# Performance work log

Hardware: AMD Instinct MI355X
Metric: run time of the kernel (lower is better)

Reference implementation:

```python
import jax, jax.numpy as jnp
import numpy as np

EPS_BN = 1e-5   # torch BatchNorm1d default eps
K = 3           # de_neighbors


def conv1(x, w):
    # 1x1 Conv1d, no bias: x [B,C,N], w [O,C] -> [B,O,N]
    return jnp.einsum('oc,bcn->bon', w, x)


def bn_relu(y, g, b):
    # BatchNorm1d in training mode (batch statistics, biased variance) + ReLU
    mean = jnp.mean(y, axis=(0, 2), keepdims=True)
    var = jnp.var(y, axis=(0, 2), keepdims=True)
    yn = (y - mean) * jax.lax.rsqrt(var + EPS_BN)
    return jax.nn.relu(yn * g[None, :, None] + b[None, :, None])


def propagate(xyz1, xyz2, p1, p2, k):
    # xyz1 [B,N,3] fine coords, xyz2 [B,S,3] coarse coords,
    # p1 [B,D1,N] fine feats, p2 [B,D2,S] coarse feats -> [B,D1+D2,N]
    pts2 = p2.transpose(0, 2, 1)  # [B,S,D2]
    # squared pairwise distances [B,N,S]
    d = (jnp.sum(xyz1 ** 2, -1)[:, :, None]
         + jnp.sum(xyz2 ** 2, -1)[:, None, :]
         - 2.0 * jnp.einsum('bnc,bsc->bns', xyz1, xyz2))
    negd, idx = jax.lax.top_k(-d, k)          # k smallest distances
    dists = -negd                              # [B,N,k]
    w = 1.0 / (dists + 1e-8)
    w = w / jnp.sum(w, -1, keepdims=True)      # inverse-distance weights
    B = xyz1.shape[0]
    gathered = pts2[jnp.arange(B)[:, None, None], idx]     # [B,N,k,D2]
    interp = jnp.sum(gathered * w[..., None], axis=2)      # [B,N,D2]
    new = jnp.concatenate([p1.transpose(0, 2, 1), interp], axis=-1)
    return new.transpose(0, 2, 1)


def setup_inputs() -> dict:
    key = jax.random.key(0)
    ks = jax.random.split(key, 20)
    B = 16
    npts = [2048, 512, 128, 32, 8]
    ch = [64, 128, 256, 512, 1024]
    inp = {}
    for i in range(5):
        inp[f'xyz{i}'] = jax.random.normal(ks[i], (B, npts[i], 3), jnp.float32)
        inp[f'x{i}'] = jax.random.normal(ks[5 + i], (B, ch[i], npts[i]), jnp.float32)
    lin_dims = [1536, 1792, 1920, 1984]
    for i, dmid in enumerate(lin_dims):
        inp[f'w_lin{i}'] = jax.random.normal(ks[10 + i], (dmid, dmid), jnp.float32) * (1.0 / np.sqrt(dmid))
        inp[f'g_lin{i}'] = jnp.ones((dmid,), jnp.float32)
        inp[f'b_lin{i}'] = jnp.zeros((dmid,), jnp.float32)
    inp['w_dec0'] = jax.random.normal(ks[14], (256, 1984), jnp.float32) * (1.0 / np.sqrt(1984))
    inp['g_dec'] = jnp.ones((256,), jnp.float32)
    inp['b_dec'] = jnp.zeros((256,), jnp.float32)
    inp['w_dec1'] = jax.random.normal(ks[15], (1, 256), jnp.float32) * (1.0 / np.sqrt(256))
    return inp


def reference(xyz0, xyz1, xyz2, xyz3, xyz4,
              x0, x1, x2, x3, x4,
              w_lin0, g_lin0, b_lin0,
              w_lin1, g_lin1, b_lin1,
              w_lin2, g_lin2, b_lin2,
              w_lin3, g_lin3, b_lin3,
              w_dec0, g_dec, b_dec, w_dec1):
    # lists are reversed in forward: coarsest first
    x = x4
    x = propagate(xyz3, xyz4, x3, x, K)   # [B,1536,32]
    x = bn_relu(conv1(x, w_lin0), g_lin0, b_lin0)
    x = propagate(xyz2, xyz3, x2, x, K)   # [B,1792,128]
    x = bn_relu(conv1(x, w_lin1), g_lin1, b_lin1)
    x = propagate(xyz1, xyz2, x1, x, K)   # [B,1920,512]
    x = bn_relu(conv1(x, w_lin2), g_lin2, b_lin2)
    x = propagate(xyz0, xyz1, x0, x, K)   # [B,1984,2048]
    x = bn_relu(conv1(x, w_lin3), g_lin3, b_lin3)
    # str_dec: Linear1Layer(1984,256) -> Dropout(eval=identity) -> Conv1d(256,1)
    x = bn_relu(conv1(x, w_dec0), g_dec, b_dec)
    out = conv1(x, w_dec1)                # [B,1,N]
    return out.squeeze(1)                 # [B,N]
```

## Files before the change

kernel.cpp:

```cpp
#include <hip/hip_runtime.h>
#include <stdint.h>
#include <stddef.h>

typedef _Float16 half8 __attribute__((ext_vector_type(8)));
typedef _Float16 half4v __attribute__((ext_vector_type(4)));
typedef float f32x4 __attribute__((ext_vector_type(4)));

__device__ __forceinline__ void gload_lds16(const void* g, void* l) {
  __builtin_amdgcn_global_load_lds((const __attribute__((address_space(1))) void*)g,
                                   (__attribute__((address_space(3))) void*)l, 16, 0, 0);
}

struct TPack {
  const float* in[5];
  _Float16* out[5];
  int C[5], N[5];
  int cum[6];
};
__global__ __launch_bounds__(256) void k_transpose_all(TPack p) {
  __shared__ float tile[32][33];
  int t = blockIdx.x;
  int ti = 0;
#pragma unroll
  for (int i = 0; i < 5; ++i) if (t >= p.cum[i + 1]) ti = i + 1;
// ... 16 lines not shown
  __syncthreads();
#pragma unroll
  for (int j = 0; j < 32; j += 8) {
    int n = n0 + ty + j, c = c0 + tx;
    if (n < N && c < C) out[((size_t)b * N + n) * C + c] = (_Float16)tile[tx][ty + j];
  }
}

__global__ __launch_bounds__(256) void k_cast_pad_w(const float* __restrict__ W,
                                                    _Float16* __restrict__ Wh,
                                                    int O, int K, int Opad, int Kpad) {
  size_t i = ((size_t)blockIdx.x * 256 + threadIdx.x) * 4;
  if (i >= (size_t)Opad * Kpad) return;
  int r = (int)(i / Kpad), k = (int)(i % Kpad);
  half4v v;
#pragma unroll
  for (int j = 0; j < 4; ++j) {
    float f = (r < O && (k + j) < K) ? W[(size_t)r * K + k + j] : 0.f;
    v[j] = (_Float16)f;
  }
  *(half4v*)(Wh + i) = v;
}

struct KPack {
  const float* q[4]; const float* p[4];
  int N1[4], S[4];
  int cum[5];
  int obase[4];
};
#define KNN_INS(dd, ii) { float _d = (dd); int _i = (ii); \
  if (_d < d0)      { d2 = d1; i2 = i1; d1 = d0; i1 = i0; d0 = _d; i0 = _i; } \
  else if (_d < d1) { d2 = d1; i2 = i1; d1 = _d; i1 = _i; } \
  else if (_d < d2) { d2 = _d; i2 = _i; } }
__global__ __launch_bounds__(256) void k_knn_all(KPack kp, int4* __restrict__ idxo,
                                                 float4* __restrict__ wo) {
  __shared__ float sp[512 * 3];
  __shared__ float spp[512];
  int t = blockIdx.x;
  int st = 0;
#pragma unroll
  for (int i = 0; i < 4; ++i) if (t >= kp.cum[i + 1]) st = i + 1;
  int lb = t - kp.cum[st];
  int N1 = kp.N1[st], S = kp.S[st];
  int nb = (N1 * 4 + 255) / 256;
  int b = lb / nb;
  int xb = lb - b * nb;
  const float* p = kp.p[st];
  const float* q = kp.q[st];
  for (int i = threadIdx.x; i < S * 3; i += 256) sp[i] = p[(size_t)b * S * 3 + i];
  __syncthreads();
  for (int s = threadIdx.x; s < S; s += 256)
    spp[s] = sp[s * 3] * sp[s * 3] + sp[s * 3 + 1] * sp[s * 3 + 1] + sp[s * 3 + 2] * sp[s * 3 + 2];
  __syncthreads();
  int tt = xb * 256 + threadIdx.x;
  int n = tt >> 2, sub = tt & 3;
  if (n >= N1) return;
  const float* qp = q + ((size_t)b * N1 + n) * 3;
  float qx = qp[0], qy = qp[1], qz = qp[2];
  float qq = qx * qx + qy * qy + qz * qz;
  float d0 = 1e30f, d1 = 1e30f, d2 = 1e30f;
  int i0 = 0, i1 = 0, i2 = 0;
  int Sq = S >> 2;
  int s0 = sub * Sq;
  for (int i = 0; i < Sq; ++i) {
    int s = s0 + i;
    float d = qq + spp[s] - 2.f * (qx * sp[s * 3] + qy * sp[s * 3 + 1] + qz * sp[s * 3 + 2]);
    KNN_INS(d, s);
  }
#pragma unroll
  for (int m = 1; m <= 2; m <<= 1) {
    float rd0 = __shfl_xor(d0, m, 64), rd1 = __shfl_xor(d1, m, 64), rd2 = __shfl_xor(d2, m, 64);
    int   ri0 = __shfl_xor(i0, m, 64), ri1 = __shfl_xor(i1, m, 64), ri2 = __shfl_xor(i2, m, 64);
    KNN_INS(rd0, ri0); KNN_INS(rd1, ri1); KNN_INS(rd2, ri2);
  }
  if (sub == 0) {
    float w0 = 1.f / (d0 + 1e-8f), w1 = 1.f / (d1 + 1e-8f), w2 = 1.f / (d2 + 1e-8f);
    float wsum = w0 + w1 + w2;
    int gi = kp.obase[st] + b * N1 + n;
    idxo[gi] = make_int4(b * S + i0, b * S + i1, b * S + i2, 0);
    wo[gi] = make_float4(w0 / wsum, w1 / wsum, w2 / wsum, 0.f);
  }
}

__global__ __launch_bounds__(256) void k_bn_norm(_Float16* __restrict__ G,
                                                 const float* __restrict__ scale,
                                                 const float* __restrict__ shiftv,
                                                 size_t total8, int ld) {
  size_t i = (size_t)blockIdx.x * 256 + threadIdx.x;
  if (i >= total8) return;
  half8 v = *(half8*)&G[i * 8];
  int c0 = (int)((i * 8) % (size_t)ld);
#pragma unroll
  for (int j = 0; j < 8; ++j) {
    float f = (float)v[j] * scale[c0 + j] + shiftv[c0 + j];
    v[j] = (_Float16)fmaxf(f, 0.f);
  }
  *(half8*)&G[i * 8] = v;
}


__global__ __launch_bounds__(256) void k_gemm_anorm(const _Float16* __restrict__ A,
                                                    const float* __restrict__ scale,
                                                    const float* __restrict__ shift,
                                                    int apply_nr,
                                                    const _Float16* __restrict__ W,
                                                    _Float16* __restrict__ Cout,
                                                    int K, int lda, int ldb, int ldc) {
  __shared__ __align__(16) _Float16 lA[128 * 64];
  __shared__ __align__(16) _Float16 lB[128 * 64];
  int tid = threadIdx.x;
  int m0 = blockIdx.x * 128;
  int o0 = blockIdx.y * 128;
  int lane = tid & 63, wv = tid >> 6;
  int wm = (wv & 1) * 64, wo = (wv >> 1) * 64;
  int lr = lane & 15, lq = lane >> 4;
  int trow = tid >> 3;
  int tsegl = (((tid & 7) ^ (trow & 7))) * 8;
  int sw = lr & 7;

  f32x4 acc[4][4];
#pragma unroll
  for (int mi = 0; mi < 4; ++mi)
#pragma unroll
    for (int oi = 0; oi < 4; ++oi)
      acc[mi][oi] = (f32x4){0.f, 0.f, 0.f, 0.f};

  const _Float16* gA = A + (size_t)(m0 + trow) * lda + tsegl;
  const _Float16* gB = W + (size_t)(o0 + trow) * ldb + tsegl;

  for (int k0 = 0; k0 < K; k0 += 64) {
#pragma unroll
    for (int i = 0; i < 4; ++i)
      gload_lds16(gB + (size_t)(32 * i) * ldb + k0, lB + ((size_t)i * 256 + tid) * 8);
    if (apply_nr) {
      float sc[8], sh[8];
#pragma unroll
      for (int j = 0; j < 8; ++j) { sc[j] = scale[k0 + tsegl + j]; sh[j] = shift[k0 + tsegl + j]; }
#pragma unroll
      for (int i = 0; i < 4; ++i) {
        half8 v = *(const half8*)(gA + (size_t)(32 * i) * lda + k0);
        half8 o;
#pragma unroll
        for (int j = 0; j < 8; ++j)
          o[j] = (_Float16)fmaxf((float)v[j] * sc[j] + sh[j], 0.f);
        *(half8*)&lA[((size_t)i * 256 + tid) * 8] = o;
      }
    } else {
#pragma unroll
      for (int i = 0; i < 4; ++i)
        gload_lds16(gA + (size_t)(32 * i) * lda + k0, lA + ((size_t)i * 256 + tid) * 8);
    }
    __syncthreads();
#pragma unroll
    for (int ks = 0; ks < 64; ks += 32) {
      half8 af[4], bf[4];
#pragma unroll
      for (int mi = 0; mi < 4; ++mi)
        af[mi] = *(const half8*)&lA[(wm + mi * 16 + lr) * 64 + ((((ks >> 3) + lq) ^ sw)) * 8];
#pragma unroll
      for (int oi = 0; oi < 4; ++oi)
        bf[oi] = *(const half8*)&lB[(wo + oi * 16 + lr) * 64 + ((((ks >> 3) + lq) ^ sw)) * 8];
#pragma unroll
      for (int mi = 0; mi < 4; ++mi)
#pragma unroll
        for (int oi = 0; oi < 4; ++oi)
          acc[mi][oi] = __builtin_amdgcn_mfma_f32_16x16x32_f16(af[mi], bf[oi], acc[mi][oi], 0, 0, 0);
    }
    __syncthreads();
  }

#pragma unroll
  for (int mi = 0; mi < 4; ++mi)
#pragma unroll
    for (int oi = 0; oi < 4; ++oi) {
      int col = o0 + wo + oi * 16 + lr;
      int rowb = m0 + wm + mi * 16 + lq * 4;
#pragma unroll
      for (int r = 0; r < 4; ++r)
        Cout[(size_t)(rowb + r) * ldc + col] = (_Float16)acc[mi][oi][r];
    }
}

__global__ __launch_bounds__(256) void k_gemm_yis(const _Float16* __restrict__ A,
                                                  const _Float16* __restrict__ W,
                                                  const _Float16* __restrict__ Z,
                                                  const int4* __restrict__ idxb,
                                                  const float4* __restrict__ wb,
                                                  _Float16* __restrict__ Y,
                                                  float* __restrict__ sum,
                                                  float* __restrict__ sumsq,
                                                  int K, int lda, int ldb, int ldy,
                                                  int ldz, int zcol0) {
  __shared__ __align__(16) _Float16 lsm[2 * 128 * 64];
  __shared__ int4 sIdx[128];
  __shared__ float4 sWt[128];
  __shared__ float sStat[256];
  _Float16* lA = lsm;
  _Float16* lB = lsm + 128 * 64;
  int tid = threadIdx.x;
  int m0 = blockIdx.x * 128;
  int o0 = blockIdx.y * 128;
  if (tid < 128) {
    sIdx[tid] = idxb[m0 + tid];
    sWt[tid] = wb[m0 + tid];
  }
  sStat[tid] = 0.f;
  int lane = tid & 63, wv = tid >> 6;
  int wm = (wv & 1) * 64, wo = (wv >> 1) * 64;
  int lr = lane & 15, lq = lane >> 4;
  int trow = tid >> 3;
  int tsegl = (((tid & 7) ^ (trow & 7))) * 8;
  int sw = lr & 7;

  f32x4 acc[4][4];
#pragma unroll
  for (int mi = 0; mi < 4; ++mi)
#pragma unroll
    for (int oi = 0; oi < 4; ++oi)
      acc[mi][oi] = (f32x4){0.f, 0.f, 0.f, 0.f};

  const _Float16* gA = A + (size_t)(m0 + trow) * lda + tsegl;
  const _Float16* gB = W + (size_t)(o0 + trow) * ldb + tsegl;

  for (int k0 = 0; k0 < K; k0 += 64) {
#pragma unroll
    for (int i = 0; i < 4; ++i) {
      gload_lds16(gA + (size_t)(32 * i) * lda + k0, lA + ((size_t)i * 256 + tid) * 8);
      gload_lds16(gB + (size_t)(32 * i) * ldb + k0, lB + ((size_t)i * 256 + tid) * 8);
    }
    __syncthreads();
#pragma unroll
    for (int ks = 0; ks < 64; ks += 32) {
      half8 af[4], bf[4];
#pragma unroll
      for (int mi = 0; mi < 4; ++mi)
        af[mi] = *(const half8*)&lA[(wm + mi * 16 + lr) * 64 + ((((ks >> 3) + lq) ^ sw)) * 8];
#pragma unroll
      for (int oi = 0; oi < 4; ++oi)
        bf[oi] = *(const half8*)&lB[(wo + oi * 16 + lr) * 64 + ((((ks >> 3) + lq) ^ sw)) * 8];
#pragma unroll
      for (int mi = 0; mi < 4; ++mi)
#pragma unroll
        for (int oi = 0; oi < 4; ++oi)
          acc[mi][oi] = __builtin_amdgcn_mfma_f32_16x16x32_f16(af[mi], bf[oi], acc[mi][oi], 0, 0, 0);
    }
    __syncthreads();
  }

#pragma unroll
  for (int mi = 0; mi < 4; ++mi)
#pragma unroll
    for (int oi = 0; oi < 4; ++oi)
#pragma unroll
      for (int r = 0; r < 4; ++r)
        lsm[(wm + mi * 16 + lq * 4 + r) * 128 + (wo + oi * 16 + lr)] = (_Float16)acc[mi][oi][r];
  __syncthreads();

  int tcol = (tid & 15) * 8;
  int rbase = tid >> 4;
  float s8[8], q8[8];
#pragma unroll
  for (int j = 0; j < 8; ++j) { s8[j] = 0.f; q8[j] = 0.f; }
#pragma unroll
  for (int i = 0; i < 8; ++i) {
    int row = rbase + i * 16;
    int4 id = sIdx[row];
    float4 w = sWt[row];
    half8 y = *(half8*)&lsm[row * 128 + tcol];
    int zc = zcol0 + o0 + tcol;
    half8 a  = *(const half8*)&Z[(size_t)id.x * ldz + zc];
    half8 b2 = *(const half8*)&Z[(size_t)id.y * ldz + zc];
    half8 c2 = *(const half8*)&Z[(size_t)id.z * ldz + zc];
    half8 o;
#pragma unroll
    for (int j = 0; j < 8; ++j) {
      float v = (float)y[j] + w.x * (float)a[j] + w.y * (float)b2[j] + w.z * (float)c2[j];
      o[j] = (_Float16)v;
      s8[j] += v; q8[j] += v * v;
    }
    *(half8*)&Y[(size_t)(m0 + row) * ldy + o0 + tcol] = o;
  }
#pragma unroll
  for (int j = 0; j < 8; ++j) {
    atomicAdd(&sStat[tcol + j], s8[j]);
    atomicAdd(&sStat[128 + tcol + j], q8[j]);
  }
  __syncthreads();
  if (tid < 128) {
    atomicAdd(&sum[o0 + tid], sStat[tid]);
    atomicAdd(&sumsq[o0 + tid], sStat[128 + tid]);
  }
}

__global__ __launch_bounds__(256) void k_gemm_dec_acc(const _Float16* __restrict__ A,
                                                      const float* __restrict__ sumc,
                                                      const float* __restrict__ sumsqc,
                                                      const float* __restrict__ g,
                                                      const float* __restrict__ b,
                                                      float invM, int c0, int Oglob,
                                                      const _Float16* __restrict__ W,
                                                      float* __restrict__ D,
                                                      int K, int lda, int ldb, int ldc,
                                                      int accum, int do_stats,
                                                      float* __restrict__ dsum,
                                                      float* __restrict__ dsumsq) {
  __shared__ __align__(16) _Float16 lA[128 * 64];
  __shared__ __align__(16) _Float16 lB[128 * 64];
  __shared__ float sScale[2048];
  __shared__ float sShift[2048];
  __shared__ float sStat[256];
  int tid = threadIdx.x;
  int m0 = blockIdx.x * 128;
  int o0 = blockIdx.y * 128;
  for (int c = tid; c < K; c += 256) {
    int gc = c0 + c;
    float sc = 0.f, sh = 0.f;
    if (gc < Oglob) {
      float mean = sumc[c] * invM;
      float var = sumsqc[c] * invM - mean * mean;
      sc = g[gc] * rsqrtf(var + 1e-5f);
      sh = b[gc] - mean * sc;
    }
    sScale[c] = sc; sShift[c] = sh;
  }
  sStat[tid] = 0.f;
  __syncthreads();

  int lane = tid & 63, wv = tid >> 6;
  int wm = (wv & 1) * 64, wo = (wv >> 1) * 64;
  int lr = lane & 15, lq = lane >> 4;
  int trow = tid >> 3;
  int tsegl = (((tid & 7) ^ (trow & 7))) * 8;
  int sw = lr & 7;

  f32x4 acc[4][4];
#pragma unroll
  for (int mi = 0; mi < 4; ++mi)
#pragma unroll
    for (int oi = 0; oi < 4; ++oi)
      acc[mi][oi] = (f32x4){0.f, 0.f, 0.f, 0.f};

  const _Float16* gA = A + (size_t)(m0 + trow) * lda + tsegl;
  const _Float16* gB = W + (size_t)(o0 + trow) * ldb + tsegl;

  for (int k0 = 0; k0 < K; k0 += 64) {
#pragma unroll
    for (int i = 0; i < 4; ++i)
      gload_lds16(gB + (size_t)(32 * i) * ldb + k0, lB + ((size_t)i * 256 + tid) * 8);
    float sc[8], sh[8];
#pragma unroll
    for (int j = 0; j < 8; ++j) { sc[j] = sScale[k0 + tsegl + j]; sh[j] = sShift[k0 + tsegl + j]; }
#pragma unroll
    for (int i = 0; i < 4; ++i) {
      half8 v = *(const half8*)(gA + (size_t)(32 * i) * lda + k0);
      half8 o;
#pragma unroll
      for (int j = 0; j < 8; ++j)
        o[j] = (_Float16)fmaxf((float)v[j] * sc[j] + sh[j], 0.f);
      *(half8*)&lA[((size_t)i * 256 + tid) * 8] = o;
    }
    __syncthreads();
#pragma unroll
    for (int ks = 0; ks < 64; ks += 32) {
      half8 af[4], bf[4];
#pragma unroll
      for (int mi = 0; mi < 4; ++mi)
        af[mi] = *(const half8*)&lA[(wm + mi * 16 + lr) * 64 + ((((ks >> 3) + lq) ^ sw)) * 8];
#pragma unroll
      for (int oi = 0; oi < 4; ++oi)
        bf[oi] = *(const half8*)&lB[(wo + oi * 16 + lr) * 64 + ((((ks >> 3) + lq) ^ sw)) * 8];
#pragma unroll
      for (int mi = 0; mi < 4; ++mi)
#pragma unroll
        for (int oi = 0; oi < 4; ++oi)
          acc[mi][oi] = __builtin_amdgcn_mfma_f32_16x16x32_f16(af[mi], bf[oi], acc[mi][oi], 0, 0, 0);
    }
    __syncthreads();
  }

  float ps[4], pq[4];
#pragma unroll
  for (int oi = 0; oi < 4; ++oi) { ps[oi] = 0.f; pq[oi] = 0.f; }
#pragma unroll
  for (int mi = 0; mi < 4; ++mi)
#pragma unroll
    for (int oi = 0; oi < 4; ++oi) {
      int col = o0 + wo + oi * 16 + lr;
      int rowb = m0 + wm + mi * 16 + lq * 4;
#pragma unroll
      for (int r = 0; r < 4; ++r) {
        size_t idx = (size_t)(rowb + r) * ldc + col;
        float v = acc[mi][oi][r];
        if (accum) v += D[idx];
        D[idx] = v;
        if (do_stats) { ps[oi] += v; pq[oi] += v * v; }
      }
    }
  if (do_stats) {
#pragma unroll
    for (int oi = 0; oi < 4; ++oi) {
      int tc = wo + oi * 16 + lr;
      atomicAdd(&sStat[tc], ps[oi]);
      atomicAdd(&sStat[128 + tc], pq[oi]);
    }
    __syncthreads();
    if (tid < 128) {
      atomicAdd(&dsum[o0 + tid], sStat[tid]);
      atomicAdd(&dsumsq[o0 + tid], sStat[128 + tid]);
    }
  }
}

__global__ __launch_bounds__(256) void k_bn_finalize(const float* __restrict__ sum,
                                                     const float* __restrict__ sumsq,
                                                     const float* __restrict__ g, const float* __restrict__ b,
                                                     float* __restrict__ scale, float* __restrict__ shiftv,
                                                     int O, int Opad, float invM) {
  int c = blockIdx.x * 256 + threadIdx.x;
  if (c >= Opad) return;
  if (c < O) {
    float mean = sum[c] * invM;
    float var = sumsq[c] * invM - mean * mean;
    float sc = g[c] * rsqrtf(var + 1e-5f);
    scale[c] = sc;
    shiftv[c] = b[c] - mean * sc;
  } else {
    scale[c] = 0.f;
    shiftv[c] = 0.f;
  }
}

__global__ __launch_bounds__(256) void k_final_dot_f32(const float* __restrict__ H,
                                                       const float* __restrict__ w,
                                                       const float* __restrict__ scale,
                                                       const float* __restrict__ shiftv,
                                                       float* __restrict__ out, int Mtot) {
  int lane = threadIdx.x & 63, wv = threadIdx.x >> 6;
  int r = blockIdx.x * 4 + wv;
  if (r >= Mtot) return;
  const float* h = H + (size_t)r * 256;
  float s = 0.f;
  for (int c = lane; c < 256; c += 64)
    s += fmaxf(h[c] * scale[c] + shiftv[c], 0.f) * w[c];
#pragma unroll
  for (int o = 32; o > 0; o >>= 1) s += __shfl_down(s, o, 64);
  if (lane == 0) out[r] = s;
}

extern "C" void kernel_launch(void* const* d_in, const int* in_sizes, int n_in,
                              void* d_out, int out_size, void* d_ws, size_t ws_size,
                              hipStream_t stream) {
  (void)in_sizes; (void)n_in; (void)out_size;
  const int B = 16;
  const float* xyzs[5]; const float* xs[5];
  for (int i = 0; i < 5; ++i) { xyzs[i] = (const float*)d_in[2 * i]; xs[i] = (const float*)d_in[2 * i + 1]; }
  const float* wlin[4] = {(const float*)d_in[10], (const float*)d_in[13], (const float*)d_in[16], (const float*)d_in[19]};
  const float* glin[4] = {(const float*)d_in[11], (const float*)d_in[14], (const float*)d_in[17], (const float*)d_in[20]};
  const float* blin[4] = {(const float*)d_in[12], (const float*)d_in[15], (const float*)d_in[18], (const float*)d_in[21]};
  const float* wdec0 = (const float*)d_in[22];
  const float* gdec  = (const float*)d_in[23];
  const float* bdec  = (const float*)d_in[24];
  const float* wdec1 = (const float*)d_in[25];
  float* outp = (float*)d_out;

  const int ch[5] = {64, 128, 256, 512, 1024};
  const int np[5] = {2048, 512, 128, 32, 8};

  char* base = (char*)d_ws;
  size_t off = 0;
  auto alloc = [&](size_t bytes) -> char* {
    char* p = base + off;
    off += (bytes + 255) & ~(size_t)255;
    return p;
  };

  _Float16* Wbuf = (_Float16*)alloc((size_t)2048 * 1984 * 2);
  _Float16* Wdec = (_Float16*)alloc((size_t)256 * 2048 * 2);
  _Float16* tT[5];
  for (int i = 0; i < 5; ++i) tT[i] = (_Float16*)alloc((size_t)B * np[i] * ch[i] * 2);
  int4* idxAll = (int4*)alloc(43520 * sizeof(int4));
  float4* wbAll = (float4*)alloc(43520 * sizeof(float4));
  float* statsPool = (float*)alloc(8 * 2 * 2048 * sizeof(float));
  float* scaleA = (float*)alloc(2048 * sizeof(float));
  float* shiftA = (float*)alloc(2048 * sizeof(float));
  float* scaleC = (float*)alloc(2048 * sizeof(float));
  float* shiftC = (float*)alloc(2048 * sizeof(float));
  _Float16* Zreg = (_Float16*)alloc((size_t)8192 * 2048 * 2);
  float* D = (float*)alloc((size_t)32768 * 256 * 4);
  size_t ybytes_chunk = 40370176;
  size_t ybytes_full = (size_t)32768 * 2048 * 2;
  int use_full = (ws_size >= off + ybytes_full + 256);
  char* Yreg = alloc(use_full ? ybytes_full : ybytes_chunk);
  _Float16* Y0 = (_Float16*)Yreg;
  _Float16* Y1 = (_Float16*)(Yreg + (size_t)512 * 1536 * 2);
  _Float16* Y2 = (_Float16*)(Yreg + (size_t)(512 * 1536 + 2048 * 1792) * 2);
  _Float16* Ychunk = (_Float16*)Yreg;
  _Float16* Y3full = (_Float16*)Yreg;
  if (off > ws_size) return;

  hipMemsetAsync(statsPool, 0, 8 * 2 * 2048 * sizeof(float), stream);

  {
    TPack p;
    int cum = 0;
    for (int i = 0; i < 5; ++i) {
      p.in[i] = xs[i]; p.out[i] = tT[i]; p.C[i] = ch[i]; p.N[i] = np[i];
      p.cum[i] = cum;
      cum += (ch[i] / 32) * ((np[i] + 31) / 32) * B;
    }
    p.cum[5] = cum;
    k_transpose_all<<<cum, dim3(32, 8), 0, stream>>>(p);
  }
  {
    size_t tot4 = (size_t)256 * 2048 / 4;
    k_cast_pad_w<<<dim3((unsigned)((tot4 + 255) / 256)), 256, 0, stream>>>(wdec0, Wdec, 256, 1984, 256, 2048);
  }

  const int N1s[4] = {32, 128, 512, 2048};
  const int Ss[4]  = {8, 32, 128, 512};
  const int C1s[4] = {512, 256, 128, 64};
  const int C2s[4] = {1024, 1536, 1792, 1920};
  const int Os[4]  = {1536, 1792, 1920, 1984};
  const int obase[4] = {0, 512, 2560, 10752};
  _Float16* Ys[3] = {Y0, Y1, Y2};

  {
    KPack kp;
    int cum = 0;
    for (int st = 0; st < 4; ++st) {
      kp.q[st] = xyzs[3 - st]; kp.p[st] = xyzs[4 - st];
      kp.N1[st] = N1s[st]; kp.S[st] = Ss[st];
      kp.cum[st] = cum;
      cum += ((N1s[st] * 4 + 255) / 256) * B;
      kp.obase[st] = obase[st];
    }
    kp.cum[4] = cum;
    k_knn_all<<<cum, 256, 0, stream>>>(kp, idxAll, wbAll);
  }

  for (int st = 0; st < 3; ++st) {
    int N1 = N1s[st], C1 = C1s[st], C2 = C2s[st], O = Os[st];
    int Ktot = C1 + C2;
    int M = B * N1, Msrc = B * Ss[st];
    const _Float16* H = (st == 0) ? tT[4] : Ys[st - 1];
    _Float16* Y = Ys[st];
    float* sum = statsPool + st * 2 * 2048;
    float* sumsq = sum + 2048;

    size_t wt = (size_t)O * Ktot / 4;
    k_cast_pad_w<<<(unsigned)((wt + 255) / 256), 256, 0, stream>>>(wlin[st], Wbuf, O, Ktot, O, Ktot);

    k_gemm_anorm<<<dim3(Msrc / 128, O / 128), 256, 0, stream>>>(H, scaleA, shiftA, st != 0,
                                                                Wbuf + C1, Zreg, C2, C2, Ktot, O);
    k_gemm_yis<<<dim3(M / 128, O / 128), 256, 0, stream>>>(tT[3 - st], Wbuf, Zreg,
                                                           idxAll + obase[st], wbAll + obase[st],
                                                           Y, sum, sumsq,
                                                           C1, C1, Ktot, O, O, 0);
    k_bn_finalize<<<(O + 255) / 256, 256, 0, stream>>>(sum, sumsq, glin[st], blin[st], scaleA, shiftA, O, O, 1.f / M);
  }

  {
    int C1 = 64, C2 = 1920, O = 1984, M = 32768, Msrc = 8192;
    int Ktot = 1984;
    size_t wt = (size_t)2048 * Ktot / 4;
    k_cast_pad_w<<<(unsigned)((wt + 255) / 256), 256, 0, stream>>>(wlin[3], Wbuf, O, Ktot, 2048, Ktot);

    size_t tot8 = (size_t)Msrc * 1920 / 8;
    k_bn_norm<<<(unsigned)((tot8 + 255) / 256), 256, 0, stream>>>(Y2, scaleA, shiftA, tot8, 1920);
    k_gemm_anorm<<<dim3(Msrc / 128, 16), 256, 0, stream>>>(Y2, scaleA, shiftA, 0,
                                                           Wbuf + C1, Zreg, C2, C2, Ktot, 2048);

    float* dsum = statsPool + 7 * 2 * 2048;
    float* dsumsq = dsum + 2048;
    if (use_full) {
      float* sum = statsPool + 3 * 2 * 2048;
      float* sumsq = sum + 2048;
      k_gemm_yis<<<dim3(M / 128, 16), 256, 0, stream>>>(tT[0], Wbuf, Zreg,
                                                        idxAll + obase[3], wbAll + obase[3],
                                                        Y3full, sum, sumsq,
                                                        C1, C1, Ktot, 2048, 2048, 0);
      k_gemm_dec_acc<<<dim3(M / 128, 2), 256, 0, stream>>>(Y3full, sum, sumsq,
                                                           glin[3], blin[3], 1.f / M, 0, O,
                                                           Wdec, D, 2048, 2048, 2048, 256,
                                                           0, 1, dsum, dsumsq);
    } else {
      for (int c0 = 0; c0 < 2048; c0 += 512) {
        float* sum = statsPool + (3 + c0 / 512) * 2 * 2048;
        float* sumsq = sum + 2048;
        k_gemm_yis<<<dim3(M / 128, 4), 256, 0, stream>>>(tT[0], Wbuf + (size_t)c0 * Ktot, Zreg,
                                                         idxAll + obase[3], wbAll + obase[3],
                                                         Ychunk, sum, sumsq,
                                                         C1, C1, Ktot, 512, 2048, c0);
        k_gemm_dec_acc<<<dim3(M / 128, 2), 256, 0, stream>>>(Ychunk, sum, sumsq,
                                                             glin[3], blin[3], 1.f / M, c0, O,
                                                             Wdec + c0, D, 512, 512, 2048, 256,
                                                             c0 != 0, c0 == 1536, dsum, dsumsq);
      }
    }
  }

  {
    int M = 32768, O = 256;
    float* dsum = statsPool + 7 * 2 * 2048;
    float* dsumsq = dsum + 2048;
    k_bn_finalize<<<1, 256, 0, stream>>>(dsum, dsumsq, gdec, bdec, scaleC, shiftC, O, O, 1.f / M);
    k_final_dot_f32<<<M / 4, 256, 0, stream>>>(D, wdec1, scaleC, shiftC, outp, M);
  }
}
```

Measured before the change: 703.2 us.

## Fold BN finalize into consumers, normalize in place, swizzle final GEMM block order

Drops the separate BN finalize kernels. Scale and shift are now recomputed from the raw sums inside a new in-place normalize kernel and inside the final dot kernel. The normalize-on-load path in the source-feature GEMM is replaced by a standalone normalize pass followed by a plain GEMM that streams A with direct-to-LDS loads. A block-index swizzle is added to the largest yis GEMM so that groups of output tiles share the same A rows in cache. This removes launches and per-element ALU work from the GEMM, but adds an extra read and write pass over the intermediate activations and redundant rsqrt work per element.

```diff
diff --git a/kernel.cpp b/kernel.cpp
--- a/kernel.cpp
+++ b/kernel.cpp
@@ -122,27 +122,30 @@
   }
 }
 
-__global__ __launch_bounds__(256) void k_bn_norm(_Float16* __restrict__ G,
-                                                 const float* __restrict__ scale,
-                                                 const float* __restrict__ shiftv,
-                                                 size_t total8, int ld) {
+__global__ __launch_bounds__(256) void k_bn_norm2(_Float16* __restrict__ G,
+                                                  const float* __restrict__ sum,
+                                                  const float* __restrict__ sumsq,
+                                                  const float* __restrict__ g,
+                                                  const float* __restrict__ b,
+                                                  float invM, size_t total8, int ld) {
   size_t i = (size_t)blockIdx.x * 256 + threadIdx.x;
   if (i >= total8) return;
   half8 v = *(half8*)&G[i * 8];
   int c0 = (int)((i * 8) % (size_t)ld);
 #pragma unroll
   for (int j = 0; j < 8; ++j) {
-    float f = (float)v[j] * scale[c0 + j] + shiftv[c0 + j];
-    v[j] = (_Float16)fmaxf(f, 0.f);
+    int c = c0 + j;
+    float mean = sum[c] * invM;
+    float var = sumsq[c] * invM - mean * mean;
+    float sc = g[c] * rsqrtf(var + 1e-5f);
+    float sh = b[c] - mean * sc;
+    v[j] = (_Float16)fmaxf((float)v[j] * sc + sh, 0.f);
   }
   *(half8*)&G[i * 8] = v;
 }
 
 
-__global__ __launch_bounds__(256) void k_gemm_anorm(const _Float16* __restrict__ A,
-                                                    const float* __restrict__ scale,
-                                                    const float* __restrict__ shift,
-                                                    int apply_nr,
+__global__ __launch_bounds__(256) void k_gemm_plain(const _Float16* __restrict__ A,
                                                     const _Float16* __restrict__ W,
                                                     _Float16* __restrict__ Cout,
                                                     int K, int lda, int ldb, int ldc) {
@@ -170,25 +173,9 @@
 
   for (int k0 = 0; k0 < K; k0 += 64) {
 #pragma unroll
-    for (int i = 0; i < 4; ++i)
+    for (int i = 0; i < 4; ++i) {
+      gload_lds16(gA + (size_t)(32 * i) * lda + k0, lA + ((size_t)i * 256 + tid) * 8);
       gload_lds16(gB + (size_t)(32 * i) * ldb + k0, lB + ((size_t)i * 256 + tid) * 8);
-    if (apply_nr) {
-      float sc[8], sh[8];
-#pragma unroll
-      for (int j = 0; j < 8; ++j) { sc[j] = scale[k0 + tsegl + j]; sh[j] = shift[k0 + tsegl + j]; }
-#pragma unroll
-      for (int i = 0; i < 4; ++i) {
-        half8 v = *(const half8*)(gA + (size_t)(32 * i) * lda + k0);
-        half8 o;
-#pragma unroll
-        for (int j = 0; j < 8; ++j)
-          o[j] = (_Float16)fmaxf((float)v[j] * sc[j] + sh[j], 0.f);
-        *(half8*)&lA[((size_t)i * 256 + tid) * 8] = o;
-      }
-    } else {
-#pragma unroll
-      for (int i = 0; i < 4; ++i)
-        gload_lds16(gA + (size_t)(32 * i) * lda + k0, lA + ((size_t)i * 256 + tid) * 8);
     }
     __syncthreads();
 #pragma unroll
@@ -230,7 +217,7 @@
                                                   float* __restrict__ sum,
                                                   float* __restrict__ sumsq,
                                                   int K, int lda, int ldb, int ldy,
-                                                  int ldz, int zcol0) {
+                                                  int ldz, int zcol0, int swz) {
   __shared__ __align__(16) _Float16 lsm[2 * 128 * 64];
   __shared__ int4 sIdx[128];
   __shared__ float4 sWt[128];
@@ -238,8 +225,15 @@
   _Float16* lA = lsm;
   _Float16* lB = lsm + 128 * 64;
   int tid = threadIdx.x;
-  int m0 = blockIdx.x * 128;
-  int o0 = blockIdx.y * 128;
+  int m0, o0;
+  if (swz) {
+    int bid = blockIdx.y * gridDim.x + blockIdx.x;
+    int o = (bid & 7) + ((bid >> 11) << 3);
+    int m = (bid >> 3) & 255;
+    m0 = m * 128; o0 = o * 128;
+  } else {
+    m0 = blockIdx.x * 128; o0 = blockIdx.y * 128;
+  }
   if (tid < 128) {
     sIdx[tid] = idxb[m0 + tid];
     sWt[tid] = wb[m0 + tid];
@@ -451,37 +445,26 @@
   }
 }
 
-__global__ __launch_bounds__(256) void k_bn_finalize(const float* __restrict__ sum,
-                                                     const float* __restrict__ sumsq,
-                                                     const float* __restrict__ g, const float* __restrict__ b,
-                                                     float* __restrict__ scale, float* __restrict__ shiftv,
-                                                     int O, int Opad, float invM) {
-  int c = blockIdx.x * 256 + threadIdx.x;
-  if (c >= Opad) return;
-  if (c < O) {
-    float mean = sum[c] * invM;
-    float var = sumsq[c] * invM - mean * mean;
-    float sc = g[c] * rsqrtf(var + 1e-5f);
-    scale[c] = sc;
-    shiftv[c] = b[c] - mean * sc;
-  } else {
-    scale[c] = 0.f;
-    shiftv[c] = 0.f;
-  }
-}
-
-__global__ __launch_bounds__(256) void k_final_dot_f32(const float* __restrict__ H,
-                                                       const float* __restrict__ w,
-                                                       const float* __restrict__ scale,
-                                                       const float* __restrict__ shiftv,
-                                                       float* __restrict__ out, int Mtot) {
+__global__ __launch_bounds__(256) void k_final_dot2(const float* __restrict__ H,
+                                                    const float* __restrict__ w,
+                                                    const float* __restrict__ dsum,
+                                                    const float* __restrict__ dsumsq,
+                                                    const float* __restrict__ g,
+                                                    const float* __restrict__ b,
+                                                    float invM,
+                                                    float* __restrict__ out, int Mtot) {
   int lane = threadIdx.x & 63, wv = threadIdx.x >> 6;
   int r = blockIdx.x * 4 + wv;
   if (r >= Mtot) return;
   const float* h = H + (size_t)r * 256;
   float s = 0.f;
-  for (int c = lane; c < 256; c += 64)
-    s += fmaxf(h[c] * scale[c] + shiftv[c], 0.f) * w[c];
+  for (int c = lane; c < 256; c += 64) {
+    float mean = dsum[c] * invM;
+    float var = dsumsq[c] * invM - mean * mean;
+    float sc = g[c] * rsqrtf(var + 1e-5f);
+    float sh = b[c] - mean * sc;
+    s += fmaxf(h[c] * sc + sh, 0.f) * w[c];
+  }
 #pragma unroll
   for (int o = 32; o > 0; o >>= 1) s += __shfl_down(s, o, 64);
   if (lane == 0) out[r] = s;
@@ -521,10 +504,6 @@
   int4* idxAll = (int4*)alloc(43520 * sizeof(int4));
   float4* wbAll = (float4*)alloc(43520 * sizeof(float4));
   float* statsPool = (float*)alloc(8 * 2 * 2048 * sizeof(float));
-  float* scaleA = (float*)alloc(2048 * sizeof(float));
-  float* shiftA = (float*)alloc(2048 * sizeof(float));
-  float* scaleC = (float*)alloc(2048 * sizeof(float));
-  float* shiftC = (float*)alloc(2048 * sizeof(float));
   _Float16* Zreg = (_Float16*)alloc((size_t)8192 * 2048 * 2);
   float* D = (float*)alloc((size_t)32768 * 256 * 4);
   size_t ybytes_chunk = 40370176;
@@ -582,7 +561,6 @@
     int N1 = N1s[st], C1 = C1s[st], C2 = C2s[st], O = Os[st];
     int Ktot = C1 + C2;
     int M = B * N1, Msrc = B * Ss[st];
-    const _Float16* H = (st == 0) ? tT[4] : Ys[st - 1];
     _Float16* Y = Ys[st];
     float* sum = statsPool + st * 2 * 2048;
     float* sumsq = sum + 2048;
@@ -590,13 +568,23 @@
     size_t wt = (size_t)O * Ktot / 4;
     k_cast_pad_w<<<(unsigned)((wt + 255) / 256), 256, 0, stream>>>(wlin[st], Wbuf, O, Ktot, O, Ktot);
 
-    k_gemm_anorm<<<dim3(Msrc / 128, O / 128), 256, 0, stream>>>(H, scaleA, shiftA, st != 0,
-                                                                Wbuf + C1, Zreg, C2, C2, Ktot, O);
+    const _Float16* H;
+    if (st == 0) {
+      H = tT[4];
+    } else {
+      _Float16* Hn = Ys[st - 1];
+      float* psum = statsPool + (st - 1) * 2 * 2048;
+      size_t tot8 = (size_t)Msrc * C2 / 8;
+      k_bn_norm2<<<(unsigned)((tot8 + 255) / 256), 256, 0, stream>>>(Hn, psum, psum + 2048,
+                                                                     glin[st - 1], blin[st - 1],
+                                                                     1.f / Msrc, tot8, C2);
+      H = Hn;
+    }
+    k_gemm_plain<<<dim3(Msrc / 128, O / 128), 256, 0, stream>>>(H, Wbuf + C1, Zreg, C2, C2, Ktot, O);
     k_gemm_yis<<<dim3(M / 128, O / 128), 256, 0, stream>>>(tT[3 - st], Wbuf, Zreg,
                                                            idxAll + obase[st], wbAll + obase[st],
                                                            Y, sum, sumsq,
-                                                           C1, C1, Ktot, O, O, 0);
-    k_bn_finalize<<<(O + 255) / 256, 256, 0, stream>>>(sum, sumsq, glin[st], blin[st], scaleA, shiftA, O, O, 1.f / M);
+                                                           C1, C1, Ktot, O, O, 0, 0);
   }
 
   {
@@ -605,10 +593,12 @@
     size_t wt = (size_t)2048 * Ktot / 4;
     k_cast_pad_w<<<(unsigned)((wt + 255) / 256), 256, 0, stream>>>(wlin[3], Wbuf, O, Ktot, 2048, Ktot);
 
+    float* s2 = statsPool + 2 * 2 * 2048;
     size_t tot8 = (size_t)Msrc * 1920 / 8;
-    k_bn_norm<<<(unsigned)((tot8 + 255) / 256), 256, 0, stream>>>(Y2, scaleA, shiftA, tot8, 1920);
-    k_gemm_anorm<<<dim3(Msrc / 128, 16), 256, 0, stream>>>(Y2, scaleA, shiftA, 0,
-                                                           Wbuf + C1, Zreg, C2, C2, Ktot, 2048);
+    k_bn_norm2<<<(unsigned)((tot8 + 255) / 256), 256, 0, stream>>>(Y2, s2, s2 + 2048,
+                                                                   glin[2], blin[2],
+                                                                   1.f / Msrc, tot8, 1920);
+    k_gemm_plain<<<dim3(Msrc / 128, 16), 256, 0, stream>>>(Y2, Wbuf + C1, Zreg, C2, C2, Ktot, 2048);
 
     float* dsum = statsPool + 7 * 2 * 2048;
     float* dsumsq = dsum + 2048;
@@ -618,7 +608,7 @@
       k_gemm_yis<<<dim3(M / 128, 16), 256, 0, stream>>>(tT[0], Wbuf, Zreg,
                                                         idxAll + obase[3], wbAll + obase[3],
                                                         Y3full, sum, sumsq,
-                                                        C1, C1, Ktot, 2048, 2048, 0);
+                                                        C1, C1, Ktot, 2048, 2048, 0, 1);
       k_gemm_dec_acc<<<dim3(M / 128, 2), 256, 0, stream>>>(Y3full, sum, sumsq,
                                                            glin[3], blin[3], 1.f / M, 0, O,
                                                            Wdec, D, 2048, 2048, 2048, 256,
@@ -630,7 +620,7 @@
         k_gemm_yis<<<dim3(M / 128, 4), 256, 0, stream>>>(tT[0], Wbuf + (size_t)c0 * Ktot, Zreg,
                                                          idxAll + obase[3], wbAll + obase[3],
                                                          Ychunk, sum, sumsq,
-                                                         C1, C1, Ktot, 512, 2048, c0);
+                                                         C1, C1, Ktot, 512, 2048, c0, 0);
         k_gemm_dec_acc<<<dim3(M / 128, 2), 256, 0, stream>>>(Ychunk, sum, sumsq,
                                                              glin[3], blin[3], 1.f / M, c0, O,
                                                              Wdec + c0, D, 512, 512, 2048, 256,
@@ -640,10 +630,9 @@
   }
 
   {
-    int M = 32768, O = 256;
+    int M = 32768;
     float* dsum = statsPool + 7 * 2 * 2048;
     float* dsumsq = dsum + 2048;
-    k_bn_finalize<<<1, 256, 0, stream>>>(dsum, dsumsq, gdec, bdec, scaleC, shiftC, O, O, 1.f / M);
-    k_final_dot_f32<<<M / 4, 256, 0, stream>>>(D, wdec1, scaleC, shiftC, outp, M);
-  }
-}
+    k_final_dot2<<<M / 4, 256, 0, stream>>>(D, wdec1, dsum, dsumsq, gdec, bdec, 1.f / M, outp, M);
+  }
+}
```

New measurement: 784.5 us. 11.6% more time.

## Use 64-row tiles with swizzled block order for last-layer GEMMs; fuse BN finalize

Applied to the files above, without the earlier changes.

Adds a 64x128-tile variant of the last propagate GEMM, with a block-index swizzle that groups eight output-column tiles per row strip so the A and Z gathers get L2 reuse. It also doubles the number of blocks. The decoder GEMM gets an optional swizzled block order. The final BN finalize is folded into the final dot kernel, which drops one launch. The smaller tile lowers MFMA reuse per LDS load, and the fused finalize repeats the scale computation in every block.

```diff
diff --git a/kernel.cpp b/kernel.cpp
--- a/kernel.cpp
+++ b/kernel.cpp
@@ -136,6 +136,25 @@
     v[j] = (_Float16)fmaxf(f, 0.f);
   }
   *(half8*)&G[i * 8] = v;
+}
+
+__global__ __launch_bounds__(256) void k_bn_finalize(const float* __restrict__ sum,
+                                                     const float* __restrict__ sumsq,
+                                                     const float* __restrict__ g, const float* __restrict__ b,
+                                                     float* __restrict__ scale, float* __restrict__ shiftv,
+                                                     int O, int Opad, float invM) {
+  int c = blockIdx.x * 256 + threadIdx.x;
+  if (c >= Opad) return;
+  if (c < O) {
+    float mean = sum[c] * invM;
+    float var = sumsq[c] * invM - mean * mean;
+    float sc = g[c] * rsqrtf(var + 1e-5f);
+    scale[c] = sc;
+    shiftv[c] = b[c] - mean * sc;
+  } else {
+    scale[c] = 0.f;
+    shiftv[c] = 0.f;
+  }
 }
 
 
@@ -332,6 +351,119 @@
   }
 }
 
+__global__ __launch_bounds__(256) void k_gemm_yis64(const _Float16* __restrict__ A,
+                                                    const _Float16* __restrict__ W,
+                                                    const _Float16* __restrict__ Z,
+                                                    const int4* __restrict__ idxb,
+                                                    const float4* __restrict__ wb,
+                                                    _Float16* __restrict__ Y,
+                                                    float* __restrict__ sum,
+                                                    float* __restrict__ sumsq,
+                                                    int K, int lda, int ldb, int ldy,
+                                                    int ldz) {
+  __shared__ __align__(16) _Float16 lsm[64 * 64 + 128 * 64];
+  __shared__ int4 sIdx[64];
+  __shared__ float4 sWt[64];
+  __shared__ float sStat[256];
+  _Float16* lA = lsm;
+  _Float16* lB = lsm + 64 * 64;
+  int tid = threadIdx.x;
+  int bid = blockIdx.y * gridDim.x + blockIdx.x;
+  int o0 = ((bid & 7) + ((bid >> 12) << 3)) * 128;
+  int m0 = ((bid >> 3) & 511) * 64;
+  if (tid < 64) {
+    sIdx[tid] = idxb[m0 + tid];
+    sWt[tid] = wb[m0 + tid];
+  }
+  sStat[tid] = 0.f;
+  int lane = tid & 63, wv = tid >> 6;
+  int wm = (wv & 1) * 32, wo = (wv >> 1) * 64;
+  int lr = lane & 15, lq = lane >> 4;
+  int trow = tid >> 3;
+  int tsegl = (((tid & 7) ^ (trow & 7))) * 8;
+  int sw = lr & 7;
+
+  f32x4 acc[2][4];
+#pragma unroll
+  for (int mi = 0; mi < 2; ++mi)
+#pragma unroll
+    for (int oi = 0; oi < 4; ++oi)
+      acc[mi][oi] = (f32x4){0.f, 0.f, 0.f, 0.f};
+
+  const _Float16* gA = A + (size_t)(m0 + trow) * lda + tsegl;
+  const _Float16* gB = W + (size_t)(o0 + trow) * ldb + tsegl;
+
+  for (int k0 = 0; k0 < K; k0 += 64) {
+#pragma unroll
+    for (int i = 0; i < 2; ++i)
+      gload_lds16(gA + (size_t)(32 * i) * lda + k0, lA + ((size_t)i * 256 + tid) * 8);
+#pragma unroll
+    for (int i = 0; i < 4; ++i)
+      gload_lds16(gB + (size_t)(32 * i) * ldb + k0, lB + ((size_t)i * 256 + tid) * 8);
+    __syncthreads();
+#pragma unroll
+    for (int ks = 0; ks < 64; ks += 32) {
+      half8 af[2], bf[4];
+#pragma unroll
+      for (int mi = 0; mi < 2; ++mi)
+        af[mi] = *(const half8*)&lA[(wm + mi * 16 + lr) * 64 + ((((ks >> 3) + lq) ^ sw)) * 8];
+#pragma unroll
+      for (int oi = 0; oi < 4; ++oi)
+        bf[oi] = *(const half8*)&lB[(wo + oi * 16 + lr) * 64 + ((((ks >> 3) + lq) ^ sw)) * 8];
+#pragma unroll
+      for (int mi = 0; mi < 2; ++mi)
+#pragma unroll
+        for (int oi = 0; oi < 4; ++oi)
+          acc[mi][oi] = __builtin_amdgcn_mfma_f32_16x16x32_f16(af[mi], bf[oi], acc[mi][oi], 0, 0, 0);
+    }
+    __syncthreads();
+  }
+
+#pragma unroll
+  for (int mi = 0; mi < 2; ++mi)
+#pragma unroll
+    for (int oi = 0; oi < 4; ++oi)
+#pragma unroll
+      for (int r = 0; r < 4; ++r)
+        lsm[(wm + mi * 16 + lq * 4 + r) * 128 + (wo + oi * 16 + lr)] = (_Float16)acc[mi][oi][r];
+  __syncthreads();
+
+  int tcol = (tid & 15) * 8;
+  int rbase = tid >> 4;
+  float s8[8], q8[8];
+#pragma unroll
+  for (int j = 0; j < 8; ++j) { s8[j] = 0.f; q8[j] = 0.f; }
+#pragma unroll
+  for (int i = 0; i < 4; ++i) {
+    int row = rbase + i * 16;
+    int4 id = sIdx[row];
+    float4 w = sWt[row];
+    half8 y = *(half8*)&lsm[row * 128 + tcol];
+    int zc = o0 + tcol;
+    half8 a  = *(const half8*)&Z[(size_t)id.x * ldz + zc];
+    half8 b2 = *(const half8*)&Z[(size_t)id.y * ldz + zc];
+    half8 c2 = *(const half8*)&Z[(size_t)id.z * ldz + zc];
+    half8 o;
+#pragma unroll
+    for (int j = 0; j < 8; ++j) {
+      float v = (float)y[j] + w.x * (float)a[j] + w.y * (float)b2[j] + w.z * (float)c2[j];
+      o[j] = (_Float16)v;
+      s8[j] += v; q8[j] += v * v;
+    }
+    *(half8*)&Y[(size_t)(m0 + row) * ldy + o0 + tcol] = o;
+  }
+#pragma unroll
+  for (int j = 0; j < 8; ++j) {
+    atomicAdd(&sStat[tcol + j], s8[j]);
+    atomicAdd(&sStat[128 + tcol + j], q8[j]);
+  }
+  __syncthreads();
+  if (tid < 128) {
+    atomicAdd(&sum[o0 + tid], sStat[tid]);
+    atomicAdd(&sumsq[o0 + tid], sStat[128 + tid]);
+  }
+}
+
 __global__ __launch_bounds__(256) void k_gemm_dec_acc(const _Float16* __restrict__ A,
                                                       const float* __restrict__ sumc,
                                                       const float* __restrict__ sumsqc,
@@ -341,7 +473,7 @@
                                                       const _Float16* __restrict__ W,
                                                       float* __restrict__ D,
                                                       int K, int lda, int ldb, int ldc,
-                                                      int accum, int do_stats,
+                                                      int accum, int do_stats, int swz,
                                                       float* __restrict__ dsum,
                                                       float* __restrict__ dsumsq) {
   __shared__ __align__(16) _Float16 lA[128 * 64];
@@ -350,8 +482,15 @@
   __shared__ float sShift[2048];
   __shared__ float sStat[256];
   int tid = threadIdx.x;
-  int m0 = blockIdx.x * 128;
-  int o0 = blockIdx.y * 128;
+  int m0, o0;
+  if (swz) {
+    int bid = blockIdx.y * gridDim.x + blockIdx.x;
+    int mlow = bid & 7, oo = (bid >> 3) & 1, mhigh = bid >> 4;
+    m0 = (mhigh * 8 + mlow) * 128;
+    o0 = oo * 128;
+  } else {
+    m0 = blockIdx.x * 128; o0 = blockIdx.y * 128;
+  }
   for (int c = tid; c < K; c += 256) {
     int gc = c0 + c;
     float sc = 0.f, sh = 0.f;
@@ -451,37 +590,32 @@
   }
 }
 
-__global__ __launch_bounds__(256) void k_bn_finalize(const float* __restrict__ sum,
-                                                     const float* __restrict__ sumsq,
-                                                     const float* __restrict__ g, const float* __restrict__ b,
-                                                     float* __restrict__ scale, float* __restrict__ shiftv,
-                                                     int O, int Opad, float invM) {
-  int c = blockIdx.x * 256 + threadIdx.x;
-  if (c >= Opad) return;
-  if (c < O) {
-    float mean = sum[c] * invM;
-    float var = sumsq[c] * invM - mean * mean;
+__global__ __launch_bounds__(256) void k_final_dot2(const float* __restrict__ H,
+                                                    const float* __restrict__ w,
+                                                    const float* __restrict__ dsum,
+                                                    const float* __restrict__ dsumsq,
+                                                    const float* __restrict__ g,
+                                                    const float* __restrict__ b,
+                                                    float invM,
+                                                    float* __restrict__ out, int Mtot) {
+  __shared__ float sSc[256], sSh[256];
+  int tid = threadIdx.x;
+  {
+    int c = tid;
+    float mean = dsum[c] * invM;
+    float var = dsumsq[c] * invM - mean * mean;
     float sc = g[c] * rsqrtf(var + 1e-5f);
-    scale[c] = sc;
-    shiftv[c] = b[c] - mean * sc;
-  } else {
-    scale[c] = 0.f;
-    shiftv[c] = 0.f;
-  }
-}
-
-__global__ __launch_bounds__(256) void k_final_dot_f32(const float* __restrict__ H,
-                                                       const float* __restrict__ w,
-                                                       const float* __restrict__ scale,
-                                                       const float* __restrict__ shiftv,
-                                                       float* __restrict__ out, int Mtot) {
-  int lane = threadIdx.x & 63, wv = threadIdx.x >> 6;
+    sSc[c] = sc;
+    sSh[c] = b[c] - mean * sc;
+  }
+  __syncthreads();
+  int lane = tid & 63, wv = tid >> 6;
   int r = blockIdx.x * 4 + wv;
   if (r >= Mtot) return;
   const float* h = H + (size_t)r * 256;
   float s = 0.f;
   for (int c = lane; c < 256; c += 64)
-    s += fmaxf(h[c] * scale[c] + shiftv[c], 0.f) * w[c];
+    s += fmaxf(h[c] * sSc[c] + sSh[c], 0.f) * w[c];
 #pragma unroll
   for (int o = 32; o > 0; o >>= 1) s += __shfl_down(s, o, 64);
   if (lane == 0) out[r] = s;
@@ -523,8 +657,6 @@
   float* statsPool = (float*)alloc(8 * 2 * 2048 * sizeof(float));
   float* scaleA = (float*)alloc(2048 * sizeof(float));
   float* shiftA = (float*)alloc(2048 * sizeof(float));
-  float* scaleC = (float*)alloc(2048 * sizeof(float));
-  float* shiftC = (float*)alloc(2048 * sizeof(float));
   _Float16* Zreg = (_Float16*)alloc((size_t)8192 * 2048 * 2);
   float* D = (float*)alloc((size_t)32768 * 256 * 4);
   size_t ybytes_chunk = 40370176;
@@ -615,14 +747,14 @@
     if (use_full) {
       float* sum = statsPool + 3 * 2 * 2048;
       float* sumsq = sum + 2048;
-      k_gemm_yis<<<dim3(M / 128, 16), 256, 0, stream>>>(tT[0], Wbuf, Zreg,
-                                                        idxAll + obase[3], wbAll + obase[3],
-                                                        Y3full, sum, sumsq,
-                                                        C1, C1, Ktot, 2048, 2048, 0);
-      k_gemm_dec_acc<<<dim3(M / 128, 2), 256, 0, stream>>>(Y3full, sum, sumsq,
-                                                           glin[3], blin[3], 1.f / M, 0, O,
-                                                           Wdec, D, 2048, 2048, 2048, 256,
-                                                           0, 1, dsum, dsumsq);
+      k_gemm_yis64<<<dim3(512, 16), 256, 0, stream>>>(tT[0], Wbuf, Zreg,
+                                                      idxAll + obase[3], wbAll + obase[3],
+                                                      Y3full, sum, sumsq,
+                                                      C1, C1, Ktot, 2048, 2048);
+      k_gemm_dec_acc<<<dim3(256, 2), 256, 0, stream>>>(Y3full, sum, sumsq,
+                                                       glin[3], blin[3], 1.f / M, 0, O,
+                                                       Wdec, D, 2048, 2048, 2048, 256,
+                                                       0, 1, 1, dsum, dsumsq);
     } else {
       for (int c0 = 0; c0 < 2048; c0 += 512) {
         float* sum = statsPool + (3 + c0 / 512) * 2 * 2048;
@@ -634,16 +766,15 @@
         k_gemm_dec_acc<<<dim3(M / 128, 2), 256, 0, stream>>>(Ychunk, sum, sumsq,
                                                              glin[3], blin[3], 1.f / M, c0, O,
                                                              Wdec + c0, D, 512, 512, 2048, 256,
-                                                             c0 != 0, c0 == 1536, dsum, dsumsq);
+                                                             c0 != 0, c0 == 1536, 0, dsum, dsumsq);
       }
     }
   }
 
   {
-    int M = 32768, O = 256;
+    int M = 32768;
     float* dsum = statsPool + 7 * 2 * 2048;
     float* dsumsq = dsum + 2048;
-    k_bn_finalize<<<1, 256, 0, stream>>>(dsum, dsumsq, gdec, bdec, scaleC, shiftC, O, O, 1.f / M);
-    k_final_dot_f32<<<M / 4, 256, 0, stream>>>(D, wdec1, scaleC, shiftC, outp, M);
-  }
-}
+    k_final_dot2<<<M / 4, 256, 0, stream>>>(D, wdec1, dsum, dsumsq, gdec, bdec, 1.f / M, outp, M);
+  }
+}
```

Result: slower. 774.4 us (+10.1%).

## Swizzle block order in last-stage GEMMs and fuse BN finalize and normalize passes

Applied to the files above, without the earlier changes.

Adds an optional block-index swizzle to the final-stage yis and decoder GEMMs so that consecutive workgroups share A rows and output-column tiles, aiming to improve L2 reuse. The separate BN normalize pass over Y2 is removed, and normalization is applied inside the A-load of the anorm GEMM instead. The decoder BN finalize kernel is folded into the final dot kernel, which saves two launches and one extra pass over memory. The swizzle hardcodes a grid shape of 256x16 or 256x2, so it only holds for M=32768.

```diff
diff --git a/kernel.cpp b/kernel.cpp
--- a/kernel.cpp
+++ b/kernel.cpp
@@ -138,6 +138,25 @@
   *(half8*)&G[i * 8] = v;
 }
 
+__global__ __launch_bounds__(256) void k_bn_finalize(const float* __restrict__ sum,
+                                                     const float* __restrict__ sumsq,
+                                                     const float* __restrict__ g, const float* __restrict__ b,
+                                                     float* __restrict__ scale, float* __restrict__ shiftv,
+                                                     int O, int Opad, float invM) {
+  int c = blockIdx.x * 256 + threadIdx.x;
+  if (c >= Opad) return;
+  if (c < O) {
+    float mean = sum[c] * invM;
+    float var = sumsq[c] * invM - mean * mean;
+    float sc = g[c] * rsqrtf(var + 1e-5f);
+    scale[c] = sc;
+    shiftv[c] = b[c] - mean * sc;
+  } else {
+    scale[c] = 0.f;
+    shiftv[c] = 0.f;
+  }
+}
+
 
 __global__ __launch_bounds__(256) void k_gemm_anorm(const _Float16* __restrict__ A,
                                                     const float* __restrict__ scale,
@@ -230,7 +249,7 @@
                                                   float* __restrict__ sum,
                                                   float* __restrict__ sumsq,
                                                   int K, int lda, int ldb, int ldy,
-                                                  int ldz, int zcol0) {
+                                                  int ldz, int zcol0, int swz) {
   __shared__ __align__(16) _Float16 lsm[2 * 128 * 64];
   __shared__ int4 sIdx[128];
   __shared__ float4 sWt[128];
@@ -238,8 +257,15 @@
   _Float16* lA = lsm;
   _Float16* lB = lsm + 128 * 64;
   int tid = threadIdx.x;
-  int m0 = blockIdx.x * 128;
-  int o0 = blockIdx.y * 128;
+  int m0, o0;
+  if (swz) {
+    int bid = blockIdx.y * gridDim.x + blockIdx.x;
+    int o = (bid & 7) + ((bid >> 11) << 3);
+    int m = (bid >> 3) & 255;
+    m0 = m * 128; o0 = o * 128;
+  } else {
+    m0 = blockIdx.x * 128; o0 = blockIdx.y * 128;
+  }
   if (tid < 128) {
     sIdx[tid] = idxb[m0 + tid];
     sWt[tid] = wb[m0 + tid];
@@ -341,7 +367,7 @@
                                                       const _Float16* __restrict__ W,
                                                       float* __restrict__ D,
                                                       int K, int lda, int ldb, int ldc,
-                                                      int accum, int do_stats,
+                                                      int accum, int do_stats, int swz,
                                                       float* __restrict__ dsum,
                                                       float* __restrict__ dsumsq) {
   __shared__ __align__(16) _Float16 lA[128 * 64];
@@ -350,8 +376,15 @@
   __shared__ float sShift[2048];
   __shared__ float sStat[256];
   int tid = threadIdx.x;
-  int m0 = blockIdx.x * 128;
-  int o0 = blockIdx.y * 128;
+  int m0, o0;
+  if (swz) {
+    int bid = blockIdx.y * gridDim.x + blockIdx.x;
+    int mlow = bid & 7, oo = (bid >> 3) & 1, mhigh = bid >> 4;
+    m0 = (mhigh * 8 + mlow) * 128;
+    o0 = oo * 128;
+  } else {
+    m0 = blockIdx.x * 128; o0 = blockIdx.y * 128;
+  }
   for (int c = tid; c < K; c += 256) {
     int gc = c0 + c;
     float sc = 0.f, sh = 0.f;
@@ -451,37 +484,32 @@
   }
 }
 
-__global__ __launch_bounds__(256) void k_bn_finalize(const float* __restrict__ sum,
-                                                     const float* __restrict__ sumsq,
-                                                     const float* __restrict__ g, const float* __restrict__ b,
-                                                     float* __restrict__ scale, float* __restrict__ shiftv,
-                                                     int O, int Opad, float invM) {
-  int c = blockIdx.x * 256 + threadIdx.x;
-  if (c >= Opad) return;
-  if (c < O) {
-    float mean = sum[c] * invM;
-    float var = sumsq[c] * invM - mean * mean;
+__global__ __launch_bounds__(256) void k_final_dot2(const float* __restrict__ H,
+                                                    const float* __restrict__ w,
+                                                    const float* __restrict__ dsum,
+                                                    const float* __restrict__ dsumsq,
+                                                    const float* __restrict__ g,
+                                                    const float* __restrict__ b,
+                                                    float invM,
+                                                    float* __restrict__ out, int Mtot) {
+  __shared__ float sSc[256], sSh[256];
+  int tid = threadIdx.x;
+  {
+    int c = tid;
+    float mean = dsum[c] * invM;
+    float var = dsumsq[c] * invM - mean * mean;
     float sc = g[c] * rsqrtf(var + 1e-5f);
-    scale[c] = sc;
-    shiftv[c] = b[c] - mean * sc;
-  } else {
-    scale[c] = 0.f;
-    shiftv[c] = 0.f;
-  }
-}
-
-__global__ __launch_bounds__(256) void k_final_dot_f32(const float* __restrict__ H,
-                                                       const float* __restrict__ w,
-                                                       const float* __restrict__ scale,
-                                                       const float* __restrict__ shiftv,
-                                                       float* __restrict__ out, int Mtot) {
-  int lane = threadIdx.x & 63, wv = threadIdx.x >> 6;
+    sSc[c] = sc;
+    sSh[c] = b[c] - mean * sc;
+  }
+  __syncthreads();
+  int lane = tid & 63, wv = tid >> 6;
   int r = blockIdx.x * 4 + wv;
   if (r >= Mtot) return;
   const float* h = H + (size_t)r * 256;
   float s = 0.f;
   for (int c = lane; c < 256; c += 64)
-    s += fmaxf(h[c] * scale[c] + shiftv[c], 0.f) * w[c];
+    s += fmaxf(h[c] * sSc[c] + sSh[c], 0.f) * w[c];
 #pragma unroll
   for (int o = 32; o > 0; o >>= 1) s += __shfl_down(s, o, 64);
   if (lane == 0) out[r] = s;
@@ -523,8 +551,6 @@
   float* statsPool = (float*)alloc(8 * 2 * 2048 * sizeof(float));
   float* scaleA = (float*)alloc(2048 * sizeof(float));
   float* shiftA = (float*)alloc(2048 * sizeof(float));
-  float* scaleC = (float*)alloc(2048 * sizeof(float));
-  float* shiftC = (float*)alloc(2048 * sizeof(float));
   _Float16* Zreg = (_Float16*)alloc((size_t)8192 * 2048 * 2);
   float* D = (float*)alloc((size_t)32768 * 256 * 4);
   size_t ybytes_chunk = 40370176;
@@ -595,7 +621,7 @@
     k_gemm_yis<<<dim3(M / 128, O / 128), 256, 0, stream>>>(tT[3 - st], Wbuf, Zreg,
                                                            idxAll + obase[st], wbAll + obase[st],
                                                            Y, sum, sumsq,
-                                                           C1, C1, Ktot, O, O, 0);
+                                                           C1, C1, Ktot, O, O, 0, 0);
     k_bn_finalize<<<(O + 255) / 256, 256, 0, stream>>>(sum, sumsq, glin[st], blin[st], scaleA, shiftA, O, O, 1.f / M);
   }
 
@@ -605,9 +631,7 @@
     size_t wt = (size_t)2048 * Ktot / 4;
     k_cast_pad_w<<<(unsigned)((wt + 255) / 256), 256, 0, stream>>>(wlin[3], Wbuf, O, Ktot, 2048, Ktot);
 
-    size_t tot8 = (size_t)Msrc * 1920 / 8;
-    k_bn_norm<<<(unsigned)((tot8 + 255) / 256), 256, 0, stream>>>(Y2, scaleA, shiftA, tot8, 1920);
-    k_gemm_anorm<<<dim3(Msrc / 128, 16), 256, 0, stream>>>(Y2, scaleA, shiftA, 0,
+    k_gemm_anorm<<<dim3(Msrc / 128, 16), 256, 0, stream>>>(Y2, scaleA, shiftA, 1,
                                                            Wbuf + C1, Zreg, C2, C2, Ktot, 2048);
 
     float* dsum = statsPool + 7 * 2 * 2048;
@@ -615,14 +639,14 @@
     if (use_full) {
       float* sum = statsPool + 3 * 2 * 2048;
       float* sumsq = sum + 2048;
-      k_gemm_yis<<<dim3(M / 128, 16), 256, 0, stream>>>(tT[0], Wbuf, Zreg,
-                                                        idxAll + obase[3], wbAll + obase[3],
-                                                        Y3full, sum, sumsq,
-                                                        C1, C1, Ktot, 2048, 2048, 0);
-      k_gemm_dec_acc<<<dim3(M / 128, 2), 256, 0, stream>>>(Y3full, sum, sumsq,
-                                                           glin[3], blin[3], 1.f / M, 0, O,
-                                                           Wdec, D, 2048, 2048, 2048, 256,
-                                                           0, 1, dsum, dsumsq);
+      k_gemm_yis<<<dim3(256, 16), 256, 0, stream>>>(tT[0], Wbuf, Zreg,
+                                                    idxAll + obase[3], wbAll + obase[3],
+                                                    Y3full, sum, sumsq,
+                                                    C1, C1, Ktot, 2048, 2048, 0, 1);
+      k_gemm_dec_acc<<<dim3(256, 2), 256, 0, stream>>>(Y3full, sum, sumsq,
+                                                       glin[3], blin[3], 1.f / M, 0, O,
+                                                       Wdec, D, 2048, 2048, 2048, 256,
+                                                       0, 1, 1, dsum, dsumsq);
     } else {
       for (int c0 = 0; c0 < 2048; c0 += 512) {
         float* sum = statsPool + (3 + c0 / 512) * 2 * 2048;
@@ -630,20 +654,19 @@
         k_gemm_yis<<<dim3(M / 128, 4), 256, 0, stream>>>(tT[0], Wbuf + (size_t)c0 * Ktot, Zreg,
                                                          idxAll + obase[3], wbAll + obase[3],
                                                          Ychunk, sum, sumsq,
-                                                         C1, C1, Ktot, 512, 2048, c0);
+                                                         C1, C1, Ktot, 512, 2048, c0, 0);
         k_gemm_dec_acc<<<dim3(M / 128, 2), 256, 0, stream>>>(Ychunk, sum, sumsq,
                                                              glin[3], blin[3], 1.f / M, c0, O,
                                                              Wdec + c0, D, 512, 512, 2048, 256,
-                                                             c0 != 0, c0 == 1536, dsum, dsumsq);
+                                                             c0 != 0, c0 == 1536, 0, dsum, dsumsq);
       }
     }
   }
 
   {
-    int M = 32768, O = 256;
+    int M = 32768;
     float* dsum = statsPool + 7 * 2 * 2048;
     float* dsumsq = dsum + 2048;
-    k_bn_finalize<<<1, 256, 0, stream>>>(dsum, dsumsq, gdec, bdec, scaleC, shiftC, O, O, 1.f / M);
-    k_final_dot_f32<<<M / 4, 256, 0, stream>>>(D, wdec1, scaleC, shiftC, outp, M);
-  }
-}
+    k_final_dot2<<<M / 4, 256, 0, stream>>>(D, wdec1, dsum, dsumsq, gdec, bdec, 1.f / M, outp, M);
+  }
+}
```

New measurement: 667.4 us, median of 2. -5.1%, faster.
